# Kernel tuning notes

Measured on AMD Instinct MI355X. Metric: run time of the kernel, lower is better.

Reference implementation:

```python
import jax, jax.numpy as jnp
import numpy as np

B, N, D = 1, 65536, 1024
H = 512
R = 16  # num_regions
C = 2   # num_classes

def _gelu(x):
    return jax.nn.gelu(x, approximate=False)  # torch nn.GELU default is exact erf

def setup_inputs() -> dict:
    key = jax.random.key(0)
    ks = jax.random.split(key, 16)
    s = 0.02
    return {
        "embeddings": jax.random.normal(ks[0], (B, N, D), dtype=jnp.float32),
        # region_encoder: Linear(D,H) + GELU (dropout=0 in eval)
        "W1": jax.random.normal(ks[1], (D, H), dtype=jnp.float32) * s,
        "b1": jnp.zeros((H,), dtype=jnp.float32),
        # region_attention: Linear(H,H//2) -> tanh -> Linear(H//2,1)
        "Wa1": jax.random.normal(ks[2], (H, H // 2), dtype=jnp.float32) * s,
        "ba1": jnp.zeros((H // 2,), dtype=jnp.float32),
        "Wa2": jax.random.normal(ks[3], (H // 2, 1), dtype=jnp.float32) * s,
        "ba2": jnp.zeros((1,), dtype=jnp.float32),
        # slide_encoder: Linear(H,H) + GELU
        "Ws": jax.random.normal(ks[4], (H, H), dtype=jnp.float32) * s,
        "bs": jnp.zeros((H,), dtype=jnp.float32),
        # slide_attention
        "Wsa1": jax.random.normal(ks[5], (H, H // 2), dtype=jnp.float32) * s,
        "bsa1": jnp.zeros((H // 2,), dtype=jnp.float32),
        "Wsa2": jax.random.normal(ks[6], (H // 2, 1), dtype=jnp.float32) * s,
        "bsa2": jnp.zeros((1,), dtype=jnp.float32),
        # classifier: Linear(H,H//2) -> GELU -> Linear(H//2,C)
        "Wc1": jax.random.normal(ks[7], (H, H // 2), dtype=jnp.float32) * s,
        "bc1": jnp.zeros((H // 2,), dtype=jnp.float32),
        "Wc2": jax.random.normal(ks[8], (H // 2, C), dtype=jnp.float32) * s,
        "bc2": jnp.zeros((C,), dtype=jnp.float32),
    }

def reference(embeddings, W1, b1, Wa1, ba1, Wa2, ba2, Ws, bs, Wsa1, bsa1, Wsa2, bsa2, Wc1, bc1, Wc2, bc2):
    b, n, d = embeddings.shape
    m = n // R  # patches per region
    # coords=None path: region_ids[i] = i % R, so region r holds indices r, r+R, ...
    # Equivalent regrouping via reshape+transpose: (B, M, R, D) -> (B, R, M, D)
    x = embeddings.reshape(b, m, R, d).transpose(0, 2, 1, 3)
    # region encoder
    region_emb = _gelu(jnp.einsum('brmd,dh->brmh', x, W1) + b1)  # (B,R,M,H)
    # region attention pooling
    scores = jnp.einsum('brmk,ko->brmo', jnp.tanh(jnp.einsum('brmh,hk->brmk', region_emb, Wa1) + ba1), Wa2) + ba2  # (B,R,M,1)
    attn = jax.nn.softmax(scores, axis=2)
    region_features = jnp.sum(region_emb * attn, axis=2)  # (B,R,H)
    # slide encoder + attention pooling over regions
    slide_emb = _gelu(jnp.einsum('brh,hg->brg', region_features, Ws) + bs)  # (B,R,H)
    sattn = jnp.einsum('brk,ko->bro', jnp.tanh(jnp.einsum('brh,hk->brk', slide_emb, Wsa1) + bsa1), Wsa2) + bsa2  # (B,R,1)
    sweights = jax.nn.softmax(sattn, axis=1)
    slide_rep = jnp.sum(slide_emb * sweights, axis=1)  # (B,H)
    # classifier
    logits = _gelu(slide_rep @ Wc1 + bc1) @ Wc2 + bc2  # (B,C)
    return logits
```

## Files before the change

kernel.cpp:

```cpp
#include <hip/hip_runtime.h>

#define NTOK 65536
#define DIN  1024
#define H    512
#define HH   256
#define NREG 16
#define MPR  4096

__device__ __forceinline__ unsigned short f2bf(float f) {
  unsigned u = __float_as_uint(f);
  u += 0x7fffu + ((u >> 16) & 1u);
  return (unsigned short)(u >> 16);
}
__device__ __forceinline__ float bf2f(unsigned short s) {
  return __uint_as_float(((unsigned)s) << 16);
}
__device__ __forceinline__ float gelu_exact(float x) {
  return 0.5f * x * (1.0f + erff(x * 0.70710678118654752440f));
}
__device__ __forceinline__ unsigned cvt_pk_bf16(float lo, float hi) {
  unsigned r;
  asm("v_cvt_pk_bf16_f32 %0, %1, %2" : "=v"(r) : "v"(lo), "v"(hi));
  return r;
}
__device__ __forceinline__ unsigned short f2bf_hw(float f) {
  unsigned r;
  asm("v_cvt_pk_bf16_f32 %0, %1, %2" : "=v"(r) : "v"(f), "v"(f));
  return (unsigned short)r;
}
__device__ __forceinline__ float fast_tanh(float x) {
  float e = __expf(2.0f * x);
  return 1.0f - 2.0f * __builtin_amdgcn_rcpf(e + 1.0f);
}

typedef __attribute__((ext_vector_type(8))) short shortx8;
typedef __attribute__((ext_vector_type(4))) float floatx4;
typedef __attribute__((ext_vector_type(4))) unsigned int uintx4;

__device__ __forceinline__ void gl_lds16(const void* g, void* l) {
  __builtin_amdgcn_global_load_lds(
      (const __attribute__((address_space(1))) void*)g,
      (__attribute__((address_space(3))) void*)l, 16, 0, 0);
}

#define WAITVM(N)                                            \
  do {                                                       \
    asm volatile("s_waitcnt vmcnt(" #N ")" ::: "memory");    \
    __builtin_amdgcn_sched_barrier(0);                       \
  } while (0)
#define WAITLGKM0                                            \
  do {                                                       \
    asm volatile("s_waitcnt lgkmcnt(0)" ::: "memory");       \
    __builtin_amdgcn_sched_barrier(0);                       \
  } while (0)

__device__ __forceinline__ int swz8(int row, int seg) {
  return (row * 4 + (seg ^ ((row >> 1) & 3))) * 8;
}

__global__ __launch_bounds__(256) void k0_prep(const float* __restrict__ W1,
                                               const float* __restrict__ Wa1,
                                               unsigned short* __restrict__ W1t,
                                               unsigned short* __restrict__ Wa1t) {
  int idx = blockIdx.x * 256 + threadIdx.x;
  if (idx < DIN * H) {
    int n = idx >> 10, k = idx & 1023;
    W1t[idx] = f2bf(W1[k * H + n]);
  } else {
    int i2 = idx - DIN * H;
    int n = i2 >> 9, k = i2 & 511;
    Wa1t[i2] = f2bf(Wa1[k * HH + n]);
  }
}

__global__ __launch_bounds__(512) void k1_gemm1(const float* __restrict__ X,
                                                const unsigned short* __restrict__ W1t,
                                                const float* __restrict__ b1,
                                                unsigned short* __restrict__ Eb) {
  __shared__ __align__(16) short lA[3][128 * 32];
  __shared__ __align__(16) short lB[3][512 * 32];
  const int tid = threadIdx.x;
  const int rowBase = blockIdx.x * 128;
  const int lane = tid & 63;
  const int wave = tid >> 6;
  const int wr = wave >> 2, wc = wave & 3;
  const int l15 = lane & 15, quad = lane >> 4;

  floatx4 acc[4][8] = {};

  int offA[4], offB[8];
#pragma unroll
  for (int i = 0; i < 4; i++) offA[i] = swz8(wr * 64 + i * 16 + l15, quad);
#pragma unroll
  for (int j = 0; j < 8; j++) offB[j] = swz8(wc * 128 + j * 16 + l15, quad);

  const int arow = tid >> 2, aseg = tid & 3;
  const float* aPtr = X + (size_t)(rowBase + arow) * DIN + aseg * 8;
  const int aOff = swz8(arow, aseg);

  const unsigned short* bPS[4];
  int bDst[4];
#pragma unroll
  for (int s = 0; s < 4; s++) {
    int c = tid + s * 512;
    int n = c >> 2;
    int seg = (c & 3) ^ ((n >> 1) & 3);
    bPS[s] = W1t + (size_t)n * DIN + seg * 8;
    bDst[s] = c * 8;
  }

  {
    floatx4 p0 = __builtin_nontemporal_load((const floatx4*)aPtr);
    floatx4 p1 = __builtin_nontemporal_load((const floatx4*)aPtr + 1);
    aPtr += 32;
#pragma unroll
    for (int s = 0; s < 4; s++) gl_lds16(bPS[s], &lB[0][bDst[s]]);
#pragma unroll
    for (int s = 0; s < 4; s++) gl_lds16(bPS[s] + 32, &lB[1][bDst[s]]);
#pragma unroll
    for (int s = 0; s < 4; s++) bPS[s] += 64;
    uintx4 u;
    u[0] = cvt_pk_bf16(p0[0], p0[1]);
    u[1] = cvt_pk_bf16(p0[2], p0[3]);
    u[2] = cvt_pk_bf16(p1[0], p1[1]);
    u[3] = cvt_pk_bf16(p1[2], p1[3]);
    *(uintx4*)(&lA[0][aOff]) = u;
    WAITVM(4);
    WAITLGKM0;
    __builtin_amdgcn_s_barrier();
  }

#define K1_MFMA                                                                  \
  _Pragma("unroll") for (int i = 0; i < 4; i++)                                  \
      _Pragma("unroll") for (int j = 0; j < 8; j++)                              \
          acc[i][j] = __builtin_amdgcn_mfma_f32_16x16x32_bf16(aF[i], bF[j],      \
                                                              acc[i][j], 0, 0, 0);

#define K1_STEP(CUR, ANB, SB, DO_A, DO_B, AWAIT)                                 \
  do {                                                                           \
    shortx8 aF[4], bF[8];                                                        \
    _Pragma("unroll") for (int i = 0; i < 4; i++)                                \
        aF[i] = *(const shortx8*)(&lA[CUR][offA[i]]);                            \
    _Pragma("unroll") for (int j = 0; j < 8; j++)                                \
        bF[j] = *(const shortx8*)(&lB[CUR][offB[j]]);                            \
    floatx4 p0, p1;                                                              \
    if (DO_A) {                                                                  \
      p0 = __builtin_nontemporal_load((const floatx4*)aPtr);                     \
      p1 = __builtin_nontemporal_load((const floatx4*)aPtr + 1);                 \
      aPtr += 32;                                                                \
    }                                                                            \
    if (DO_B) {                                                                  \
      _Pragma("unroll") for (int s = 0; s < 4; s++) {                            \
        gl_lds16(bPS[s], &lB[SB][bDst[s]]);                                      \
        bPS[s] += 32;                                                            \
      }                                                                          \
    }                                                                            \
    WAITLGKM0;                                                                   \
    K1_MFMA;                                                                     \
    if (DO_A) {                                                                  \
      AWAIT;                   \
      uintx4 u;                                                                  \
      u[0] = cvt_pk_bf16(p0[0], p0[1]);                                          \
      u[1] = cvt_pk_bf16(p0[2], p0[3]);                                          \
      u[2] = cvt_pk_bf16(p1[0], p1[1]);                                          \
      u[3] = cvt_pk_bf16(p1[2], p1[3]);                                          \
      *(uintx4*)(&lA[ANB][aOff]) = u;                                            \
    }                                                                            \
    WAITLGKM0;                                                                   \
    __builtin_amdgcn_s_barrier();                                                \
  } while (0)

#pragma unroll 1
  for (int tt = 0; tt < 10; ++tt) {
    K1_STEP(0, 1, 2, true, true, WAITVM(4));
    K1_STEP(1, 2, 0, true, true, WAITVM(4));
    K1_STEP(2, 0, 1, true, true, WAITVM(4));
  }
  K1_STEP(0, 1, 2, true, false, WAITVM(0));
  {
    shortx8 aF[4], bF[8];
#pragma unroll
    for (int i = 0; i < 4; i++) aF[i] = *(const shortx8*)(&lA[1][offA[i]]);
#pragma unroll
    for (int j = 0; j < 8; j++) bF[j] = *(const shortx8*)(&lB[1][offB[j]]);
    WAITLGKM0;
    K1_MFMA;
  }
  __builtin_amdgcn_s_barrier();

  short* lE = &lB[0][0];
  const int row0 = rowBase + wr * 64;
  float bias[8];
#pragma unroll
  for (int j = 0; j < 8; j++) bias[j] = b1[wc * 128 + j * 16 + l15];
#pragma unroll
  for (int h = 0; h < 2; h++) {
    WAITLGKM0;
#pragma unroll
    for (int il = 0; il < 2; il++)
#pragma unroll
      for (int j = 0; j < 8; j++)
#pragma unroll
        for (int v = 0; v < 4; v++) {
          int r = il * 16 + quad * 4 + v;
          int col = j * 16 + l15;
          float x = acc[2 * h + il][j][v] + bias[j];
          int chunk = (col >> 3) ^ (r & 7);
          lE[wave * 4096 + r * 128 + chunk * 8 + (col & 7)] =
              (short)f2bf_hw(gelu_exact(x));
        }
    WAITLGKM0;
#pragma unroll
    for (int rr = 0; rr < 8; rr++) {
      int r = rr * 4 + quad;
      int chunk = l15 ^ (r & 7);
      shortx8 val = *(const shortx8*)(&lE[wave * 4096 + r * 128 + chunk * 8]);
      *(shortx8*)(&Eb[(size_t)(row0 + h * 32 + r) * H + wc * 128 + l15 * 8]) = val;
    }
  }
}

__global__ __launch_bounds__(512) void k2_gemm2(const unsigned short* __restrict__ Eb,
                                                const unsigned short* __restrict__ Wa1t,
                                                const float* __restrict__ ba1,
                                                const float* __restrict__ Wa2,
                                                float* __restrict__ scores) {
  __shared__ __align__(16) short lA[3][128 * 32];
  __shared__ __align__(16) short lB[3][256 * 32];
  __shared__ float part[4][128];
  const int tid = threadIdx.x;
  const int rowBase = blockIdx.x * 128;
  const int lane = tid & 63;
  const int wave = tid >> 6;
  const int wr = wave >> 2, wc = wave & 3;
  const int l15 = lane & 15, quad = lane >> 4;

  floatx4 acc[4][4] = {};

  int offA[4], offB[4];
#pragma unroll
  for (int i = 0; i < 4; i++) offA[i] = swz8(wr * 64 + i * 16 + l15, quad);
#pragma unroll
  for (int j = 0; j < 4; j++) offB[j] = swz8(wc * 64 + j * 16 + l15, quad);

  const unsigned short* aPS;
  int aDst;
  {
    int c = tid, n = c >> 2;
    int seg = (c & 3) ^ ((n >> 1) & 3);
    aPS = Eb + (size_t)(rowBase + n) * H + seg * 8;
    aDst = c * 8;
  }
  const unsigned short* bPS[2];
  int bDst[2];
#pragma unroll
  for (int s = 0; s < 2; s++) {
    int c = tid + s * 512, n = c >> 2;
    int seg = (c & 3) ^ ((n >> 1) & 3);
    bPS[s] = Wa1t + (size_t)n * H + seg * 8;
    bDst[s] = c * 8;
  }

  gl_lds16(aPS, &lA[0][aDst]);
  gl_lds16(bPS[0], &lB[0][bDst[0]]);
  gl_lds16(bPS[1], &lB[0][bDst[1]]);
  gl_lds16(aPS + 32, &lA[1][aDst]);
  gl_lds16(bPS[0] + 32, &lB[1][bDst[0]]);
  gl_lds16(bPS[1] + 32, &lB[1][bDst[1]]);
  aPS += 64; bPS[0] += 64; bPS[1] += 64;
  WAITVM(3);
  __builtin_amdgcn_s_barrier();

#define K2_MFMA                                                                  \
  _Pragma("unroll") for (int i = 0; i < 4; i++)                                  \
      _Pragma("unroll") for (int j = 0; j < 4; j++)                              \
          acc[i][j] = __builtin_amdgcn_mfma_f32_16x16x32_bf16(aF[i], bF[j],      \
                                                              acc[i][j], 0, 0, 0);

#define K2_STEP(CUR, SB, DO_B, BW)                                               \
  do {                                                                           \
    shortx8 aF[4], bF[4];                                                        \
    _Pragma("unroll") for (int i = 0; i < 4; i++)                                \
        aF[i] = *(const shortx8*)(&lA[CUR][offA[i]]);                            \
    _Pragma("unroll") for (int j = 0; j < 4; j++)                                \
        bF[j] = *(const shortx8*)(&lB[CUR][offB[j]]);                            \
    if (DO_B) {                                                                  \
      gl_lds16(aPS, &lA[SB][aDst]);                                              \
      gl_lds16(bPS[0], &lB[SB][bDst[0]]);                                        \
      gl_lds16(bPS[1], &lB[SB][bDst[1]]);                                        \
      aPS += 32; bPS[0] += 32; bPS[1] += 32;                                     \
    }                                                                            \
    WAITLGKM0;                                                                   \
    K2_MFMA;                                                                     \
    BW;                                                                          \
    __builtin_amdgcn_s_barrier();                                                \
  } while (0)

#pragma unroll 1
  for (int tt = 0; tt < 4; ++tt) {
    K2_STEP(0, 2, true, WAITVM(3));
    K2_STEP(1, 0, true, WAITVM(3));
    K2_STEP(2, 1, true, WAITVM(3));
  }
  K2_STEP(0, 2, true, WAITVM(3));
  K2_STEP(1, 0, true, WAITVM(3));
  K2_STEP(2, 1, false, WAITVM(0));
  {
    shortx8 aF[4], bF[4];
#pragma unroll
    for (int i = 0; i < 4; i++) aF[i] = *(const shortx8*)(&lA[0][offA[i]]);
#pragma unroll
    for (int j = 0; j < 4; j++) bF[j] = *(const shortx8*)(&lB[0][offB[j]]);
    WAITLGKM0;
    K2_MFMA;
  }

  float p[4][4];
#pragma unroll
  for (int i = 0; i < 4; i++)
#pragma unroll
    for (int v = 0; v < 4; v++) p[i][v] = 0.0f;
#pragma unroll
  for (int j = 0; j < 4; j++) {
    int col = wc * 64 + j * 16 + l15;
    float bias = ba1[col];
    float wa2 = Wa2[col];
#pragma unroll
    for (int i = 0; i < 4; i++)
#pragma unroll
      for (int v = 0; v < 4; v++)
        p[i][v] += fast_tanh(acc[i][j][v] + bias) * wa2;
  }
#pragma unroll
  for (int i = 0; i < 4; i++)
#pragma unroll
    for (int v = 0; v < 4; v++) {
      float t = p[i][v];
      t += __shfl_xor(t, 1, 16);
      t += __shfl_xor(t, 2, 16);
      t += __shfl_xor(t, 4, 16);
      t += __shfl_xor(t, 8, 16);
      p[i][v] = t;
    }
  if (l15 == 0) {
#pragma unroll
    for (int i = 0; i < 4; i++)
#pragma unroll
      for (int v = 0; v < 4; v++)
        part[wc][wr * 64 + i * 16 + quad * 4 + v] = p[i][v];
  }
  __syncthreads();
  if (tid < 128)
    scores[rowBase + tid] = part[0][tid] + part[1][tid] + part[2][tid] + part[3][tid];
}

__global__ __launch_bounds__(256) void k3a_softmax(const float* __restrict__ scores,
                                                   float* __restrict__ wts) {
  const int r = blockIdx.x, tid = threadIdx.x;
  __shared__ float red[256];
  float m = -1e30f;
  for (int j = tid; j < MPR; j += 256) m = fmaxf(m, scores[r + NREG * j]);
  red[tid] = m;
  __syncthreads();
  for (int s = 128; s > 0; s >>= 1) {
    if (tid < s) red[tid] = fmaxf(red[tid], red[tid + s]);
    __syncthreads();
  }
  float mx = red[0];
  __syncthreads();
  float sum = 0.0f;
  for (int j = tid; j < MPR; j += 256) sum += expf(scores[r + NREG * j] - mx);
  red[tid] = sum;
  __syncthreads();
  for (int s = 128; s > 0; s >>= 1) {
    if (tid < s) red[tid] += red[tid + s];
    __syncthreads();
  }
  float inv = 1.0f / red[0];
  for (int j = tid; j < MPR; j += 256)
    wts[r + NREG * j] = expf(scores[r + NREG * j] - mx) * inv;
}

__global__ __launch_bounds__(256) void k3b_wsum(const unsigned short* __restrict__ Eb,
                                                const float* __restrict__ wts,
                                                float* __restrict__ rf) {
  const int r = blockIdx.y;
  const int mc = blockIdx.x;
  const int tid = threadIdx.x;
  float a0 = 0.0f, a1 = 0.0f;
  for (int j = mc * 128; j < mc * 128 + 128; j++) {
    int n = r + NREG * j;
    float w = wts[n];
    unsigned v = *(const unsigned*)(Eb + (size_t)n * H + tid * 2);
    a0 += w * bf2f((unsigned short)(v & 0xffffu));
    a1 += w * bf2f((unsigned short)(v >> 16));
  }
  atomicAdd(&rf[r * H + tid * 2], a0);
  atomicAdd(&rf[r * H + tid * 2 + 1], a1);
}

__global__ __launch_bounds__(256) void k4a_slide(const float* __restrict__ rf,
                                                 const float* __restrict__ Ws,
                                                 const float* __restrict__ bs,
                                                 float* __restrict__ se) {
  const int r = blockIdx.x, tid = threadIdx.x;
  __shared__ float lrf[H];
  lrf[tid] = rf[r * H + tid];
  lrf[tid + 256] = rf[r * H + tid + 256];
  __syncthreads();
  float a0 = 0.0f, a1 = 0.0f;
  for (int k = 0; k < H; k++) {
    float x = lrf[k];
    a0 += x * Ws[k * H + tid];
    a1 += x * Ws[k * H + tid + 256];
  }
  se[r * H + tid] = gelu_exact(a0 + bs[tid]);
  se[r * H + tid + 256] = gelu_exact(a1 + bs[tid + 256]);
}

__global__ __launch_bounds__(256) void k4b_sscore(const float* __restrict__ se,
                                                  const float* __restrict__ Wsa1,
                                                  const float* __restrict__ bsa1,
                                                  const float* __restrict__ Wsa2,
                                                  const float* __restrict__ bsa2,
                                                  float* __restrict__ ss) {
  const int r = blockIdx.x, tid = threadIdx.x;
  __shared__ float lse[H];
  __shared__ float red[256];
  lse[tid] = se[r * H + tid];
  lse[tid + 256] = se[r * H + tid + 256];
  __syncthreads();
  float a = 0.0f;
  for (int k = 0; k < H; k++) a += lse[k] * Wsa1[k * HH + tid];
  red[tid] = tanhf(a + bsa1[tid]) * Wsa2[tid];
  __syncthreads();
  for (int s = 128; s > 0; s >>= 1) {
    if (tid < s) red[tid] += red[tid + s];
    __syncthreads();
  }
  if (tid == 0) ss[r] = red[0] + bsa2[0];
}

__global__ __launch_bounds__(256) void k4c_final(const float* __restrict__ se,
                                                 const float* __restrict__ ss,
                                                 const float* __restrict__ Wc1,
                                                 const float* __restrict__ bc1,
                                                 const float* __restrict__ Wc2,
                                                 const float* __restrict__ bc2,
                                                 float* __restrict__ out) {
  const int tid = threadIdx.x;
  __shared__ float srep[H];
  __shared__ float r0[256], r1[256];
  float mx = -1e30f;
  for (int i = 0; i < NREG; i++) mx = fmaxf(mx, ss[i]);
  float wv[NREG];
  float den = 0.0f;
  for (int i = 0; i < NREG; i++) { wv[i] = expf(ss[i] - mx); den += wv[i]; }
  float inv = 1.0f / den;
  float s0 = 0.0f, s1 = 0.0f;
  for (int i = 0; i < NREG; i++) {
    float w = wv[i] * inv;
    s0 += w * se[i * H + tid];
    s1 += w * se[i * H + tid + 256];
  }
  srep[tid] = s0;
  srep[tid + 256] = s1;
  __syncthreads();
  float a = 0.0f;
  for (int k = 0; k < H; k++) a += srep[k] * Wc1[k * HH + tid];
  float g = gelu_exact(a + bc1[tid]);
  r0[tid] = g * Wc2[tid * 2];
  r1[tid] = g * Wc2[tid * 2 + 1];
  __syncthreads();
  for (int s = 128; s > 0; s >>= 1) {
    if (tid < s) { r0[tid] += r0[tid + s]; r1[tid] += r1[tid + s]; }
    __syncthreads();
  }
  if (tid == 0) {
    out[0] = r0[0] + bc2[0];
    out[1] = r1[0] + bc2[1];
  }
}

extern "C" void kernel_launch(void* const* d_in, const int* in_sizes, int n_in,
                              void* d_out, int out_size, void* d_ws, size_t ws_size,
                              hipStream_t stream) {
  const float* X    = (const float*)d_in[0];
  const float* W1   = (const float*)d_in[1];
  const float* b1   = (const float*)d_in[2];
  const float* Wa1  = (const float*)d_in[3];
  const float* ba1  = (const float*)d_in[4];
  const float* Wa2  = (const float*)d_in[5];
  const float* Ws   = (const float*)d_in[7];
  const float* bs   = (const float*)d_in[8];
  const float* Wsa1 = (const float*)d_in[9];
  const float* bsa1 = (const float*)d_in[10];
  const float* Wsa2 = (const float*)d_in[11];
  const float* bsa2 = (const float*)d_in[12];
  const float* Wc1  = (const float*)d_in[13];
  const float* bc1  = (const float*)d_in[14];
  const float* Wc2  = (const float*)d_in[15];
  const float* bc2  = (const float*)d_in[16];
  float* out = (float*)d_out;

  char* ws = (char*)d_ws;
  constexpr size_t OFF_W1T  = 0;
  constexpr size_t OFF_WA1T = OFF_W1T + (size_t)H * DIN * 2;
  constexpr size_t OFF_EB   = OFF_WA1T + (size_t)HH * H * 2;
  constexpr size_t OFF_SC   = OFF_EB + (size_t)NTOK * H * 2;
  constexpr size_t OFF_RF   = OFF_SC + (size_t)NTOK * 4;
  constexpr size_t OFF_WT   = OFF_RF + (size_t)NREG * H * 4;
  constexpr size_t OFF_SE   = OFF_WT + (size_t)NTOK * 4;
  constexpr size_t OFF_SS   = OFF_SE + (size_t)NREG * H * 4;

  unsigned short* W1t  = (unsigned short*)(ws + OFF_W1T);
  unsigned short* Wa1t = (unsigned short*)(ws + OFF_WA1T);
  unsigned short* Eb   = (unsigned short*)(ws + OFF_EB);
  float* scores = (float*)(ws + OFF_SC);
  float* rf     = (float*)(ws + OFF_RF);
  float* wts    = (float*)(ws + OFF_WT);
  float* se     = (float*)(ws + OFF_SE);
  float* ssb    = (float*)(ws + OFF_SS);

  hipMemsetAsync(rf, 0, (size_t)NREG * H * 4, stream);

  k0_prep<<<(DIN * H + HH * H) / 256, 256, 0, stream>>>(W1, Wa1, W1t, Wa1t);
  k1_gemm1<<<512, 512, 0, stream>>>(X, W1t, b1, Eb);
  k2_gemm2<<<512, 512, 0, stream>>>(Eb, Wa1t, ba1, Wa2, scores);
  k3a_softmax<<<NREG, 256, 0, stream>>>(scores, wts);
  k3b_wsum<<<dim3(32, NREG), 256, 0, stream>>>(Eb, wts, rf);
  k4a_slide<<<NREG, 256, 0, stream>>>(rf, Ws, bs, se);
  k4b_sscore<<<NREG, 256, 0, stream>>>(se, Wsa1, bsa1, Wsa2, bsa2, ssb);
  k4c_final<<<1, 256, 0, stream>>>(se, ssb, Wc1, bc1, Wc2, bc2, out);
}
```

Before: 619.8 us.

## Fuse region-encoder and attention-score GEMMs, keeping the GELU tile in LDS

Merges the first GEMM (X·W1 + GELU) with the attention-score GEMM into one kernel. The bf16 GELU tile stays in shared memory and feeds the second GEMM directly, so Eb no longer has to be re-read from global memory for the score computation. It also adds s_setprio around the MFMA blocks, stores scores region-contiguously so softmax reads are coalesced, and merges the two slide-level kernels. The cost is about 146 KB of LDS per block and an unpipelined second GEMM with two barriers per K step.

```diff
diff --git a/kernel.cpp b/kernel.cpp
--- a/kernel.cpp
+++ b/kernel.cpp
@@ -73,12 +73,21 @@
   }
 }
 
-__global__ __launch_bounds__(512) void k1_gemm1(const float* __restrict__ X,
-                                                const unsigned short* __restrict__ W1t,
-                                                const float* __restrict__ b1,
-                                                unsigned short* __restrict__ Eb) {
-  __shared__ __align__(16) short lA[3][128 * 32];
-  __shared__ __align__(16) short lB[3][512 * 32];
+__global__ __launch_bounds__(512) void k12_fused(const float* __restrict__ X,
+                                                 const unsigned short* __restrict__ W1t,
+                                                 const float* __restrict__ b1,
+                                                 const unsigned short* __restrict__ Wa1t,
+                                                 const float* __restrict__ ba1,
+                                                 const float* __restrict__ Wa2,
+                                                 unsigned short* __restrict__ Eb,
+                                                 float* __restrict__ scores) {
+  __shared__ __align__(16) char sh[149504];
+  short (*lA)[128 * 32] = (short (*)[128 * 32])(sh);
+  short (*lB)[512 * 32] = (short (*)[512 * 32])(sh + 24576);
+  short* lT   = (short*)sh;
+  short* wB   = (short*)(sh + 131072);
+  float* part = (float*)(sh + 147456);
+
   const int tid = threadIdx.x;
   const int rowBase = blockIdx.x * 128;
   const int lane = tid & 63;
@@ -131,10 +140,12 @@
   }
 
 #define K1_MFMA                                                                  \
+  __builtin_amdgcn_s_setprio(1);                                                 \
   _Pragma("unroll") for (int i = 0; i < 4; i++)                                  \
       _Pragma("unroll") for (int j = 0; j < 8; j++)                              \
           acc[i][j] = __builtin_amdgcn_mfma_f32_16x16x32_bf16(aF[i], bF[j],      \
-                                                              acc[i][j], 0, 0, 0);
+                                                              acc[i][j], 0, 0, 0); \
+  __builtin_amdgcn_s_setprio(0);
 
 #define K1_STEP(CUR, ANB, SB, DO_A, DO_B, AWAIT)                                 \
   do {                                                                           \
@@ -158,7 +169,7 @@
     WAITLGKM0;                                                                   \
     K1_MFMA;                                                                     \
     if (DO_A) {                                                                  \
-      AWAIT;                   \
+      AWAIT;                                                                     \
       uintx4 u;                                                                  \
       u[0] = cvt_pk_bf16(p0[0], p0[1]);                                          \
       u[1] = cvt_pk_bf16(p0[2], p0[3]);                                          \
@@ -188,131 +199,67 @@
   }
   __builtin_amdgcn_s_barrier();
 
-  short* lE = &lB[0][0];
-  const int row0 = rowBase + wr * 64;
-  float bias[8];
-#pragma unroll
-  for (int j = 0; j < 8; j++) bias[j] = b1[wc * 128 + j * 16 + l15];
-#pragma unroll
-  for (int h = 0; h < 2; h++) {
-    WAITLGKM0;
-#pragma unroll
-    for (int il = 0; il < 2; il++)
-#pragma unroll
-      for (int j = 0; j < 8; j++)
+  {
+    const int rl0 = wr * 64;
+#pragma unroll
+    for (int j = 0; j < 8; j++) {
+      int col = wc * 128 + j * 16 + l15;
+      float bias = b1[col];
+#pragma unroll
+      for (int i = 0; i < 4; i++) {
 #pragma unroll
         for (int v = 0; v < 4; v++) {
-          int r = il * 16 + quad * 4 + v;
-          int col = j * 16 + l15;
-          float x = acc[2 * h + il][j][v] + bias[j];
-          int chunk = (col >> 3) ^ (r & 7);
-          lE[wave * 4096 + r * 128 + chunk * 8 + (col & 7)] =
+          int r = rl0 + i * 16 + quad * 4 + v;
+          float x = acc[i][j][v] + bias;
+          lT[r * 512 + (((col >> 3) ^ (r & 7)) << 3) + (col & 7)] =
               (short)f2bf_hw(gelu_exact(x));
         }
-    WAITLGKM0;
-#pragma unroll
-    for (int rr = 0; rr < 8; rr++) {
-      int r = rr * 4 + quad;
-      int chunk = l15 ^ (r & 7);
-      shortx8 val = *(const shortx8*)(&lE[wave * 4096 + r * 128 + chunk * 8]);
-      *(shortx8*)(&Eb[(size_t)(row0 + h * 32 + r) * H + wc * 128 + l15 * 8]) = val;
+      }
     }
   }
-}
-
-__global__ __launch_bounds__(512) void k2_gemm2(const unsigned short* __restrict__ Eb,
-                                                const unsigned short* __restrict__ Wa1t,
-                                                const float* __restrict__ ba1,
-                                                const float* __restrict__ Wa2,
-                                                float* __restrict__ scores) {
-  __shared__ __align__(16) short lA[3][128 * 32];
-  __shared__ __align__(16) short lB[3][256 * 32];
-  __shared__ float part[4][128];
-  const int tid = threadIdx.x;
-  const int rowBase = blockIdx.x * 128;
-  const int lane = tid & 63;
-  const int wave = tid >> 6;
-  const int wr = wave >> 2, wc = wave & 3;
-  const int l15 = lane & 15, quad = lane >> 4;
-
-  floatx4 acc[4][4] = {};
-
-  int offA[4], offB[4];
-#pragma unroll
-  for (int i = 0; i < 4; i++) offA[i] = swz8(wr * 64 + i * 16 + l15, quad);
-#pragma unroll
-  for (int j = 0; j < 4; j++) offB[j] = swz8(wc * 64 + j * 16 + l15, quad);
-
-  const unsigned short* aPS;
-  int aDst;
-  {
-    int c = tid, n = c >> 2;
-    int seg = (c & 3) ^ ((n >> 1) & 3);
-    aPS = Eb + (size_t)(rowBase + n) * H + seg * 8;
-    aDst = c * 8;
-  }
-  const unsigned short* bPS[2];
-  int bDst[2];
-#pragma unroll
-  for (int s = 0; s < 2; s++) {
-    int c = tid + s * 512, n = c >> 2;
-    int seg = (c & 3) ^ ((n >> 1) & 3);
-    bPS[s] = Wa1t + (size_t)n * H + seg * 8;
-    bDst[s] = c * 8;
-  }
-
-  gl_lds16(aPS, &lA[0][aDst]);
-  gl_lds16(bPS[0], &lB[0][bDst[0]]);
-  gl_lds16(bPS[1], &lB[0][bDst[1]]);
-  gl_lds16(aPS + 32, &lA[1][aDst]);
-  gl_lds16(bPS[0] + 32, &lB[1][bDst[0]]);
-  gl_lds16(bPS[1] + 32, &lB[1][bDst[1]]);
-  aPS += 64; bPS[0] += 64; bPS[1] += 64;
-  WAITVM(3);
-  __builtin_amdgcn_s_barrier();
-
-#define K2_MFMA                                                                  \
-  _Pragma("unroll") for (int i = 0; i < 4; i++)                                  \
-      _Pragma("unroll") for (int j = 0; j < 4; j++)                              \
-          acc[i][j] = __builtin_amdgcn_mfma_f32_16x16x32_bf16(aF[i], bF[j],      \
-                                                              acc[i][j], 0, 0, 0);
-
-#define K2_STEP(CUR, SB, DO_B, BW)                                               \
-  do {                                                                           \
-    shortx8 aF[4], bF[4];                                                        \
-    _Pragma("unroll") for (int i = 0; i < 4; i++)                                \
-        aF[i] = *(const shortx8*)(&lA[CUR][offA[i]]);                            \
-    _Pragma("unroll") for (int j = 0; j < 4; j++)                                \
-        bF[j] = *(const shortx8*)(&lB[CUR][offB[j]]);                            \
-    if (DO_B) {                                                                  \
-      gl_lds16(aPS, &lA[SB][aDst]);                                              \
-      gl_lds16(bPS[0], &lB[SB][bDst[0]]);                                        \
-      gl_lds16(bPS[1], &lB[SB][bDst[1]]);                                        \
-      aPS += 32; bPS[0] += 32; bPS[1] += 32;                                     \
-    }                                                                            \
-    WAITLGKM0;                                                                   \
-    K2_MFMA;                                                                     \
-    BW;                                                                          \
-    __builtin_amdgcn_s_barrier();                                                \
-  } while (0)
+  __syncthreads();
+
+#pragma unroll
+  for (int s = 0; s < 16; s++) {
+    int c = tid + s * 512;
+    int row = c >> 6, g = c & 63;
+    shortx8 val = *(const shortx8*)(&lT[row * 512 + ((g ^ (row & 7)) << 3)]);
+    *(shortx8*)(&Eb[(size_t)(rowBase + row) * H + g * 8]) = val;
+  }
+
+  const int wr2 = wave >> 2, wc2 = wave & 3;
+  floatx4 acc2[4][4] = {};
+  int r2[4];
+#pragma unroll
+  for (int i = 0; i < 4; i++) r2[i] = wr2 * 64 + i * 16 + l15;
+  int offB2[4];
+#pragma unroll
+  for (int j = 0; j < 4; j++) offB2[j] = swz8(wc2 * 64 + j * 16 + l15, quad);
 
 #pragma unroll 1
-  for (int tt = 0; tt < 4; ++tt) {
-    K2_STEP(0, 2, true, WAITVM(3));
-    K2_STEP(1, 0, true, WAITVM(3));
-    K2_STEP(2, 1, true, WAITVM(3));
-  }
-  K2_STEP(0, 2, true, WAITVM(3));
-  K2_STEP(1, 0, true, WAITVM(3));
-  K2_STEP(2, 1, false, WAITVM(0));
-  {
+  for (int kk = 0; kk < 16; ++kk) {
+    __syncthreads();
+#pragma unroll
+    for (int s = 0; s < 2; s++) {
+      int c = tid + s * 512;
+      int n = c >> 2;
+      int seg = (c & 3) ^ ((n >> 1) & 3);
+      gl_lds16(Wa1t + (size_t)n * H + kk * 32 + seg * 8, &wB[c * 8]);
+    }
+    __syncthreads();
     shortx8 aF[4], bF[4];
 #pragma unroll
-    for (int i = 0; i < 4; i++) aF[i] = *(const shortx8*)(&lA[0][offA[i]]);
-#pragma unroll
-    for (int j = 0; j < 4; j++) bF[j] = *(const shortx8*)(&lB[0][offB[j]]);
-    WAITLGKM0;
-    K2_MFMA;
+    for (int i = 0; i < 4; i++)
+      aF[i] = *(const shortx8*)(&lT[r2[i] * 512 + (((kk * 4 + quad) ^ (r2[i] & 7)) << 3)]);
+#pragma unroll
+    for (int j = 0; j < 4; j++) bF[j] = *(const shortx8*)(&wB[offB2[j]]);
+    __builtin_amdgcn_s_setprio(1);
+#pragma unroll
+    for (int i = 0; i < 4; i++)
+#pragma unroll
+      for (int j = 0; j < 4; j++)
+        acc2[i][j] = __builtin_amdgcn_mfma_f32_16x16x32_bf16(aF[i], bF[j], acc2[i][j], 0, 0, 0);
+    __builtin_amdgcn_s_setprio(0);
   }
 
   float p[4][4];
@@ -322,14 +269,14 @@
     for (int v = 0; v < 4; v++) p[i][v] = 0.0f;
 #pragma unroll
   for (int j = 0; j < 4; j++) {
-    int col = wc * 64 + j * 16 + l15;
+    int col = wc2 * 64 + j * 16 + l15;
     float bias = ba1[col];
     float wa2 = Wa2[col];
 #pragma unroll
     for (int i = 0; i < 4; i++)
 #pragma unroll
       for (int v = 0; v < 4; v++)
-        p[i][v] += fast_tanh(acc[i][j][v] + bias) * wa2;
+        p[i][v] += fast_tanh(acc2[i][j][v] + bias) * wa2;
   }
 #pragma unroll
   for (int i = 0; i < 4; i++)
@@ -347,19 +294,24 @@
     for (int i = 0; i < 4; i++)
 #pragma unroll
       for (int v = 0; v < 4; v++)
-        part[wc][wr * 64 + i * 16 + quad * 4 + v] = p[i][v];
-  }
-  __syncthreads();
-  if (tid < 128)
-    scores[rowBase + tid] = part[0][tid] + part[1][tid] + part[2][tid] + part[3][tid];
+        part[wc2 * 128 + wr2 * 64 + i * 16 + quad * 4 + v] = p[i][v];
+  }
+  __syncthreads();
+  if (tid < 128) {
+    float s = part[tid] + part[128 + tid] + part[256 + tid] + part[384 + tid];
+    int n = rowBase + tid;
+    scores[(n & 15) * MPR + (n >> 4)] = s;
+  }
 }
 
 __global__ __launch_bounds__(256) void k3a_softmax(const float* __restrict__ scores,
                                                    float* __restrict__ wts) {
   const int r = blockIdx.x, tid = threadIdx.x;
+  const float* sc = scores + r * MPR;
+  float* wt = wts + r * MPR;
   __shared__ float red[256];
   float m = -1e30f;
-  for (int j = tid; j < MPR; j += 256) m = fmaxf(m, scores[r + NREG * j]);
+  for (int j = tid; j < MPR; j += 256) m = fmaxf(m, sc[j]);
   red[tid] = m;
   __syncthreads();
   for (int s = 128; s > 0; s >>= 1) {
@@ -369,7 +321,7 @@
   float mx = red[0];
   __syncthreads();
   float sum = 0.0f;
-  for (int j = tid; j < MPR; j += 256) sum += expf(scores[r + NREG * j] - mx);
+  for (int j = tid; j < MPR; j += 256) sum += expf(sc[j] - mx);
   red[tid] = sum;
   __syncthreads();
   for (int s = 128; s > 0; s >>= 1) {
@@ -377,8 +329,7 @@
     __syncthreads();
   }
   float inv = 1.0f / red[0];
-  for (int j = tid; j < MPR; j += 256)
-    wts[r + NREG * j] = expf(scores[r + NREG * j] - mx) * inv;
+  for (int j = tid; j < MPR; j += 256) wt[j] = expf(sc[j] - mx) * inv;
 }
 
 __global__ __launch_bounds__(256) void k3b_wsum(const unsigned short* __restrict__ Eb,
@@ -389,8 +340,8 @@
   const int tid = threadIdx.x;
   float a0 = 0.0f, a1 = 0.0f;
   for (int j = mc * 128; j < mc * 128 + 128; j++) {
+    float w = wts[r * MPR + j];
     int n = r + NREG * j;
-    float w = wts[n];
     unsigned v = *(const unsigned*)(Eb + (size_t)n * H + tid * 2);
     a0 += w * bf2f((unsigned short)(v & 0xffffu));
     a1 += w * bf2f((unsigned short)(v >> 16));
@@ -399,12 +350,19 @@
   atomicAdd(&rf[r * H + tid * 2 + 1], a1);
 }
 
-__global__ __launch_bounds__(256) void k4a_slide(const float* __restrict__ rf,
-                                                 const float* __restrict__ Ws,
-                                                 const float* __restrict__ bs,
-                                                 float* __restrict__ se) {
+__global__ __launch_bounds__(256) void k4ab(const float* __restrict__ rf,
+                                            const float* __restrict__ Ws,
+                                            const float* __restrict__ bs,
+                                            const float* __restrict__ Wsa1,
+                                            const float* __restrict__ bsa1,
+                                            const float* __restrict__ Wsa2,
+                                            const float* __restrict__ bsa2,
+                                            float* __restrict__ se,
+                                            float* __restrict__ ss) {
   const int r = blockIdx.x, tid = threadIdx.x;
   __shared__ float lrf[H];
+  __shared__ float lse[H];
+  __shared__ float red[256];
   lrf[tid] = rf[r * H + tid];
   lrf[tid + 256] = rf[r * H + tid + 256];
   __syncthreads();
@@ -414,21 +372,12 @@
     a0 += x * Ws[k * H + tid];
     a1 += x * Ws[k * H + tid + 256];
   }
-  se[r * H + tid] = gelu_exact(a0 + bs[tid]);
-  se[r * H + tid + 256] = gelu_exact(a1 + bs[tid + 256]);
-}
-
-__global__ __launch_bounds__(256) void k4b_sscore(const float* __restrict__ se,
-                                                  const float* __restrict__ Wsa1,
-                                                  const float* __restrict__ bsa1,
-                                                  const float* __restrict__ Wsa2,
-                                                  const float* __restrict__ bsa2,
-                                                  float* __restrict__ ss) {
-  const int r = blockIdx.x, tid = threadIdx.x;
-  __shared__ float lse[H];
-  __shared__ float red[256];
-  lse[tid] = se[r * H + tid];
-  lse[tid + 256] = se[r * H + tid + 256];
+  float s0 = gelu_exact(a0 + bs[tid]);
+  float s1 = gelu_exact(a1 + bs[tid + 256]);
+  se[r * H + tid] = s0;
+  se[r * H + tid + 256] = s1;
+  lse[tid] = s0;
+  lse[tid + 256] = s1;
   __syncthreads();
   float a = 0.0f;
   for (int k = 0; k < H; k++) a += lse[k] * Wsa1[k * HH + tid];
@@ -525,11 +474,9 @@
   hipMemsetAsync(rf, 0, (size_t)NREG * H * 4, stream);
 
   k0_prep<<<(DIN * H + HH * H) / 256, 256, 0, stream>>>(W1, Wa1, W1t, Wa1t);
-  k1_gemm1<<<512, 512, 0, stream>>>(X, W1t, b1, Eb);
-  k2_gemm2<<<512, 512, 0, stream>>>(Eb, Wa1t, ba1, Wa2, scores);
+  k12_fused<<<512, 512, 0, stream>>>(X, W1t, b1, Wa1t, ba1, Wa2, Eb, scores);
   k3a_softmax<<<NREG, 256, 0, stream>>>(scores, wts);
   k3b_wsum<<<dim3(32, NREG), 256, 0, stream>>>(Eb, wts, rf);
-  k4a_slide<<<NREG, 256, 0, stream>>>(rf, Ws, bs, se);
-  k4b_sscore<<<NREG, 256, 0, stream>>>(se, Wsa1, bsa1, Wsa2, bsa2, ssb);
+  k4ab<<<NREG, 256, 0, stream>>>(rf, Ws, bs, Wsa1, bsa1, Wsa2, bsa2, se, ssb);
   k4c_final<<<1, 256, 0, stream>>>(se, ssb, Wc1, bc1, Wc2, bc2, out);
 }
```

After: 594.1 us. 1.04x faster.
